# Optimization experiments

Hardware: AMD Instinct MI355X
Metric: run time of the kernel (lower is better)

## Reference

```python
import jax, jax.numpy as jnp
import numpy as np

H = 16  # num_heads
D = 64  # head_dim (latent_dim // num_heads)


def setup_inputs() -> dict:
    key = jax.random.key(0)
    ks = jax.random.split(key, 14)
    B, L, S = 2, 1024, 4096
    input_dim, latent_dim, latent_rank = 2048, 1024, 128
    sc = 0.02
    return {
        "latent": jax.random.normal(ks[0], (B, L, latent_dim), jnp.float32),
        "x": jax.random.normal(ks[1], (B, S, input_dim), jnp.float32),
        "Wq": jax.random.normal(ks[2], (latent_dim, latent_dim), jnp.float32) * sc,
        "bq": jnp.zeros((latent_dim,), jnp.float32),
        "Wc": jax.random.normal(ks[3], (input_dim, latent_rank), jnp.float32) * sc,
        "bc": jnp.zeros((latent_rank,), jnp.float32),
        "Wk": jax.random.normal(ks[4], (latent_rank, latent_dim), jnp.float32) * sc,
        "bk": jnp.zeros((latent_dim,), jnp.float32),
        "Wv": jax.random.normal(ks[5], (latent_rank, latent_dim), jnp.float32) * sc,
        "bv": jnp.zeros((latent_dim,), jnp.float32),
        "Wo": jax.random.normal(ks[6], (latent_dim, latent_dim), jnp.float32) * sc,
        "bo": jnp.zeros((latent_dim,), jnp.float32),
    }


def reference(latent, x, Wq, bq, Wc, bc, Wk, bk, Wv, bv, Wo, bo):
    B, L, latent_dim = latent.shape
    S = x.shape[1]
    # projections
    Q = latent @ Wq + bq                      # [B, L, latent_dim]
    compressed = x @ Wc + bc                  # [B, S, latent_rank] low-rank latent
    K_full = compressed @ Wk + bk             # [B, S, latent_dim]
    V_full = compressed @ Wv + bv             # [B, S, latent_dim]
    # split heads -> [B, H, len, D]
    Qh = Q.reshape(B, L, H, D).transpose(0, 2, 1, 3)
    Kh = K_full.reshape(B, S, H, D).transpose(0, 2, 1, 3)
    Vh = V_full.reshape(B, S, H, D).transpose(0, 2, 1, 3)
    scale = 1.0 / jnp.sqrt(jnp.float32(D))
    scores = jnp.einsum("bhld,bhsd->bhls", Qh, Kh) * scale  # [B,H,L,S]
    attn = jax.nn.softmax(scores, axis=-1)
    ctx = jnp.einsum("bhls,bhsd->bhld", attn, Vh)            # [B,H,L,D]
    ctx = ctx.transpose(0, 2, 1, 3).reshape(B, L, latent_dim)
    return ctx @ Wo + bo
```

## Files before the change

kernel.cpp:

```cpp
#include <hip/hip_runtime.h>
#include <hip/hip_bf16.h>

using bf16x8  = __attribute__((ext_vector_type(8))) short;
using ushort8 = __attribute__((ext_vector_type(8))) unsigned short;
using f32x4   = __attribute__((ext_vector_type(4))) float;

#define DEVINL __device__ __forceinline__

DEVINL unsigned short f2bf(float f) {
    unsigned u = __builtin_bit_cast(unsigned, f);
    u += 0x7FFFu + ((u >> 16) & 1u);
    return (unsigned short)(u >> 16);
}

DEVINL void gload_lds16(const void* g, void* l) {
    __builtin_amdgcn_global_load_lds(
        (const __attribute__((address_space(1))) void*)g,
        (__attribute__((address_space(3))) void*)l, 16, 0, 0);
}

__global__ __launch_bounds__(256) void k_conv(const float* __restrict__ in,
                                              unsigned short* __restrict__ out,
                                              int n8) {
    int i = blockIdx.x * 256 + threadIdx.x;
    if (i >= n8) return;
    const float4* p = (const float4*)in + (size_t)i * 2;
    float4 a = p[0], b = p[1];
    ushort8 r;
    r[0] = f2bf(a.x); r[1] = f2bf(a.y); r[2] = f2bf(a.z); r[3] = f2bf(a.w);
    r[4] = f2bf(b.x); r[5] = f2bf(b.y); r[6] = f2bf(b.z); r[7] = f2bf(b.w);
    *((ushort8*)out + i) = r;
}

__global__ __launch_bounds__(256) void k_convT(const float* __restrict__ in,
                                               unsigned short* __restrict__ out,
                                               int R, int C) {
    __shared__ float t[32][33];
    int c0 = blockIdx.x * 32, r0 = blockIdx.y * 32;
    int tx = threadIdx.x, ty = threadIdx.y;
#pragma unroll
    for (int i = 0; i < 4; i++)
        t[ty + i * 8][tx] = in[(size_t)(r0 + ty + i * 8) * C + c0 + tx];
    __syncthreads();
#pragma unroll
    for (int i = 0; i < 4; i++)
        out[(size_t)(c0 + ty + i * 8) * R + r0 + tx] = f2bf(t[tx][ty + i * 8]);
}

template <int BM, int BN, int OUTBF, int BIASROW>
__global__ __launch_bounds__(256) void k_gemm(const unsigned short* __restrict__ A,
                                              const unsigned short* __restrict__ BT,
                                              const float* __restrict__ bias,
                                              void* __restrict__ Cout,
                                              int M, int N, int K, float scale) {
    constexpr int WM = BM / 2, WN = BN / 2, MI = WM / 16, NI = WN / 16;
    constexpr int CA = BM * 8 / 256, CB = BN * 8 / 256;
    __shared__ unsigned short ls[(BM + BN) * 64];
    unsigned short* lsA = ls;
    unsigned short* lsB = ls + BM * 64;
    const int tid = threadIdx.x, lane = tid & 63, w = tid >> 6;
    const int m0 = blockIdx.y * BM, n0 = blockIdx.x * BN;
    const int mw = (w >> 1) * WM, nw = (w & 1) * WN;
    const int r16 = lane & 15, g4 = lane >> 4;

    f32x4 acc[MI][NI];
#pragma unroll
    for (int a = 0; a < MI; a++)
#pragma unroll
        for (int b = 0; b < NI; b++) acc[a][b] = (f32x4){0.f, 0.f, 0.f, 0.f};

    for (int k0 = 0; k0 < K; k0 += 64) {
#pragma unroll
        for (int i = 0; i < CA; i++) {
            int ch = i * 256 + w * 64 + lane;
            int row = ch >> 3, c = ch & 7;
            gload_lds16(A + (size_t)(m0 + row) * K + k0 + c * 8,
                        lsA + (size_t)(i * 256 + w * 64) * 8);
        }
#pragma unroll
        for (int i = 0; i < CB; i++) {
            int ch = i * 256 + w * 64 + lane;
            int row = ch >> 3, c = ch & 7;
            gload_lds16(BT + (size_t)(n0 + row) * K + k0 + c * 8,
                        lsB + (size_t)(i * 256 + w * 64) * 8);
        }
        __syncthreads();
#pragma unroll
        for (int kk = 0; kk < 2; kk++) {
            bf16x8 af[MI], bfr[NI];
#pragma unroll
            for (int a = 0; a < MI; a++)
                af[a] = *(const bf16x8*)&lsA[(mw + a * 16 + r16) * 64 + kk * 32 + g4 * 8];
#pragma unroll
            for (int b = 0; b < NI; b++)
                bfr[b] = *(const bf16x8*)&lsB[(nw + b * 16 + r16) * 64 + kk * 32 + g4 * 8];
#pragma unroll
            for (int a = 0; a < MI; a++)
#pragma unroll
                for (int b = 0; b < NI; b++)
                    acc[a][b] = __builtin_amdgcn_mfma_f32_16x16x32_bf16(af[a], bfr[b], acc[a][b], 0, 0, 0);
        }
        __syncthreads();
    }
#pragma unroll
    for (int b = 0; b < NI; b++) {
        int col = n0 + nw + b * 16 + r16;
        float bvc = BIASROW ? 0.f : bias[col];
#pragma unroll
        for (int a = 0; a < MI; a++) {
#pragma unroll
            for (int r = 0; r < 4; r++) {
                int row = m0 + mw + a * 16 + g4 * 4 + r;
                float bv = BIASROW ? bias[row] : bvc;
                float v = (acc[a][b][r] + bv) * scale;
                if (OUTBF)
                    ((unsigned short*)Cout)[(size_t)row * N + col] = f2bf(v);
                else
                    ((float*)Cout)[(size_t)row * N + col] = v;
            }
        }
    }
}

__global__ __launch_bounds__(256) void k_attn(const unsigned short* __restrict__ Qb,
                                              const unsigned short* __restrict__ Kb,
                                              const unsigned short* __restrict__ VTb,
                                              float* __restrict__ ctxp,
                                              float2* __restrict__ ML) {
    constexpr int LD = 1024;
    __shared__ unsigned short lsK[2][64 * 64];
    __shared__ unsigned short lsVT[2][64 * 64];
    __shared__ unsigned short lsP[4][16 * 64];
    const int tid = threadIdx.x, lane = tid & 63, w = tid >> 6;
    const int r16 = lane & 15, g4 = lane >> 4;
    const int bh = blockIdx.y, b = bh >> 4, h = bh & 15, z = blockIdx.z;
    const int q0 = blockIdx.x * 64 + w * 16;

    const size_t qbase = ((size_t)b * 1024 + q0 + r16) * LD + h * 64;
    bf16x8 qa0 = *(const bf16x8*)&Qb[qbase + g4 * 8];
    bf16x8 qa1 = *(const bf16x8*)&Qb[qbase + 32 + g4 * 8];

    f32x4 ctxa[4];
#pragma unroll
    for (int d = 0; d < 4; d++) ctxa[d] = (f32x4){0.f, 0.f, 0.f, 0.f};
    float m_run = -1e30f, l_run = 0.f;

    const size_t kbase = (size_t)b * 4096 * LD + h * 64;
    const size_t vtbase = (size_t)bh * 64 * 4096;
    const int lrow = lane >> 3;
    const int lcol = lane & 7;

    auto STAGE = [&](int bufi, int s0) {
#pragma unroll
        for (int i = 0; i < 2; i++) {
            int row = i * 32 + w * 8 + lrow;
            int csrc = lcol ^ (row & 7);
            gload_lds16(Kb + kbase + (size_t)(s0 + row) * LD + csrc * 8,
                        &lsK[bufi][(i * 32 + w * 8) * 64]);
            gload_lds16(VTb + vtbase + (size_t)row * 4096 + s0 + csrc * 8,
                        &lsVT[bufi][(i * 32 + w * 8) * 64]);
        }
    };

    auto COMPUTE = [&](int bufi) {
        f32x4 sc[4];
#pragma unroll
        for (int ni = 0; ni < 4; ni++) sc[ni] = (f32x4){0.f, 0.f, 0.f, 0.f};
        __builtin_amdgcn_s_setprio(1);
#pragma unroll
        for (int kk = 0; kk < 2; kk++) {
            bf16x8 qa = kk ? qa1 : qa0;
#pragma unroll
            for (int ni = 0; ni < 4; ni++) {
                int row = ni * 16 + r16;
                bf16x8 kf = *(const bf16x8*)&lsK[bufi][row * 64 + (((kk * 4 + g4) ^ (row & 7)) * 8)];
                sc[ni] = __builtin_amdgcn_mfma_f32_16x16x32_bf16(kf, qa, sc[ni], 0, 0, 0);
            }
        }
        __builtin_amdgcn_s_setprio(0);

        float pmax = sc[0][0];
#pragma unroll
        for (int ni = 0; ni < 4; ni++)
#pragma unroll
            for (int r = 0; r < 4; r++)
                if (ni || r) pmax = fmaxf(pmax, sc[ni][r]);
        pmax = fmaxf(pmax, __shfl_xor(pmax, 16));
        pmax = fmaxf(pmax, __shfl_xor(pmax, 32));
        float mn = fmaxf(m_run, pmax);
        float corr = exp2f(m_run - mn);
        m_run = mn;
        float p[4][4];
        float rs = 0.f;
#pragma unroll
        for (int ni = 0; ni < 4; ni++)
#pragma unroll
            for (int r = 0; r < 4; r++) {
                p[ni][r] = exp2f(sc[ni][r] - mn);
                rs += p[ni][r];
            }
        rs += __shfl_xor(rs, 16);
        rs += __shfl_xor(rs, 32);
        l_run = l_run * corr + rs;

        float corr4[4];
#pragma unroll
        for (int r = 0; r < 4; r++) corr4[r] = __shfl(corr, g4 * 4 + r);
#pragma unroll
        for (int di = 0; di < 4; di++)
#pragma unroll
            for (int r = 0; r < 4; r++) ctxa[di][r] *= corr4[r];

#pragma unroll
        for (int ni = 0; ni < 4; ni++) {
            int sw = (ni * 2 + (g4 >> 1)) ^ (r16 & 7);
            int base = r16 * 64 + sw * 8 + (g4 & 1) * 4;
#pragma unroll
            for (int pr = 0; pr < 2; pr++) {
                unsigned u;
                asm("v_cvt_pk_bf16_f32 %0, %1, %2"
                    : "=v"(u) : "v"(p[ni][2 * pr]), "v"(p[ni][2 * pr + 1]));
                *(unsigned*)&lsP[w][base + pr * 2] = u;
            }
        }

        __builtin_amdgcn_s_setprio(1);
#pragma unroll
        for (int kk = 0; kk < 2; kk++) {
            bf16x8 pa = *(const bf16x8*)&lsP[w][r16 * 64 + (((kk * 4 + g4) ^ (r16 & 7)) * 8)];
#pragma unroll
            for (int di = 0; di < 4; di++) {
                int row = di * 16 + r16;
                bf16x8 vf = *(const bf16x8*)&lsVT[bufi][row * 64 + (((kk * 4 + g4) ^ (row & 7)) * 8)];
                ctxa[di] = __builtin_amdgcn_mfma_f32_16x16x32_bf16(pa, vf, ctxa[di], 0, 0, 0);
            }
        }
        __builtin_amdgcn_s_setprio(0);
    };

    const int s_base = z * 1024;
    STAGE(0, s_base);
    __syncthreads();
#pragma unroll 1
    for (int tt = 0; tt < 8; tt++) {
        int t0 = tt * 2;
        STAGE(1, s_base + (t0 + 1) * 64);
        COMPUTE(0);
        __syncthreads();
        if (t0 + 2 < 16) STAGE(0, s_base + (t0 + 2) * 64);
        COMPUTE(1);
        __syncthreads();
    }

    float* cp = ctxp + ((size_t)z * 2 + b) * 1024 * 1024;
#pragma unroll
    for (int r = 0; r < 4; r++) {
        int q = q0 + g4 * 4 + r;
#pragma unroll
        for (int di = 0; di < 4; di++)
            cp[(size_t)q * 1024 + h * 64 + di * 16 + r16] = ctxa[di][r];
    }
    if (g4 == 0)
        ML[(((size_t)z * 2 + b) * 16 + h) * 1024 + q0 + r16] = make_float2(m_run, l_run);
}

__global__ __launch_bounds__(256) void k_merge(const float* __restrict__ ctxp,
                                               const float2* __restrict__ ML,
                                               unsigned short* __restrict__ ctx) {
    int gid = blockIdx.x * 256 + threadIdx.x;
    int d8 = gid & 7, h = (gid >> 3) & 15, q = (gid >> 7) & 1023, b = gid >> 17;
    float m[4], l[4];
#pragma unroll
    for (int z = 0; z < 4; z++) {
        float2 e = ML[(((size_t)z * 2 + b) * 16 + h) * 1024 + q];
        m[z] = e.x; l[z] = e.y;
    }
    float M = fmaxf(fmaxf(m[0], m[1]), fmaxf(m[2], m[3]));
    float wz[4], L = 0.f;
#pragma unroll
    for (int z = 0; z < 4; z++) { wz[z] = exp2f(m[z] - M); L += wz[z] * l[z]; }
    float inv = 1.0f / L;
    float o[8];
#pragma unroll
    for (int j = 0; j < 8; j++) o[j] = 0.f;
#pragma unroll
    for (int z = 0; z < 4; z++) {
        const float4* p = (const float4*)(ctxp + ((size_t)z * 2 + b) * 1048576 +
                                          (size_t)q * 1024 + h * 64 + d8 * 8);
        float4 a = p[0], c = p[1];
        o[0] += wz[z] * a.x; o[1] += wz[z] * a.y; o[2] += wz[z] * a.z; o[3] += wz[z] * a.w;
        o[4] += wz[z] * c.x; o[5] += wz[z] * c.y; o[6] += wz[z] * c.z; o[7] += wz[z] * c.w;
    }
    ushort8 r;
#pragma unroll
    for (int j = 0; j < 8; j++) r[j] = f2bf(o[j] * inv);
    *(ushort8*)&ctx[((size_t)b * 1024 + q) * 1024 + h * 64 + d8 * 8] = r;
}

extern "C" void kernel_launch(void* const* d_in, const int* in_sizes, int n_in,
                              void* d_out, int out_size, void* d_ws, size_t ws_size,
                              hipStream_t stream) {
    const float* latent = (const float*)d_in[0];
    const float* x      = (const float*)d_in[1];
    const float* Wq     = (const float*)d_in[2];
    const float* bq     = (const float*)d_in[3];
    const float* Wc     = (const float*)d_in[4];
    const float* bc     = (const float*)d_in[5];
    const float* Wk     = (const float*)d_in[6];
    const float* bk     = (const float*)d_in[7];
    const float* Wv     = (const float*)d_in[8];
    const float* bv     = (const float*)d_in[9];
    const float* Wo     = (const float*)d_in[10];
    const float* bo     = (const float*)d_in[11];
    float* out = (float*)d_out;

    char* ws = (char*)d_ws;
    size_t off = 0;
    auto alloc = [&](size_t shorts) {
        void* p = ws + off;
        off += (shorts * 2 + 255) & ~(size_t)255;
        return (unsigned short*)p;
    };
    unsigned short* lat_bf = alloc(2097152);
    unsigned short* x_bf   = alloc(16777216);
    unsigned short* WqT    = alloc(1048576);
    unsigned short* WcT    = alloc(262144);
    unsigned short* WkT    = alloc(131072);
    unsigned short* WvT    = alloc(131072);
    unsigned short* WoT    = alloc(1048576);
    unsigned short* comp   = alloc(1048576);
    unsigned short* Qb     = alloc(2097152);
    unsigned short* Kb     = alloc(8388608);
    unsigned short* VTb    = alloc(8388608);
    unsigned short* ctxb   = alloc(2097152);
    float*          ctxp   = (float*)alloc(16777216);
    float2*         MLp    = (float2*)alloc(524288);

    dim3 tb(32, 8);
    k_conv<<<2097152 / 2048, 256, 0, stream>>>(latent, lat_bf, 2097152 / 8);
    k_conv<<<16777216 / 2048, 256, 0, stream>>>(x, x_bf, 16777216 / 8);
    k_convT<<<dim3(1024 / 32, 1024 / 32), tb, 0, stream>>>(Wq, WqT, 1024, 1024);
    k_convT<<<dim3(128 / 32, 2048 / 32), tb, 0, stream>>>(Wc, WcT, 2048, 128);
    k_convT<<<dim3(1024 / 32, 128 / 32), tb, 0, stream>>>(Wk, WkT, 128, 1024);
    k_convT<<<dim3(1024 / 32, 128 / 32), tb, 0, stream>>>(Wv, WvT, 128, 1024);
    k_convT<<<dim3(1024 / 32, 1024 / 32), tb, 0, stream>>>(Wo, WoT, 1024, 1024);

    k_gemm<64, 64, 1, 0><<<dim3(2, 128), 256, 0, stream>>>(x_bf, WcT, bc, comp, 8192, 128, 2048, 1.f);
    k_gemm<64, 64, 1, 0><<<dim3(16, 32), 256, 0, stream>>>(lat_bf, WqT, bq, Qb, 2048, 1024, 1024, 0.18033688f);
    k_gemm<128, 128, 1, 0><<<dim3(8, 64), 256, 0, stream>>>(comp, WkT, bk, Kb, 8192, 1024, 128, 1.f);
    k_gemm<64, 64, 1, 1><<<dim3(64, 16), 256, 0, stream>>>(WvT, comp, bv, VTb, 1024, 4096, 128, 1.f);
    k_gemm<64, 64, 1, 1><<<dim3(64, 16), 256, 0, stream>>>(WvT, comp + 4096 * 128, bv,
                                                           VTb + (size_t)16 * 64 * 4096, 1024, 4096, 128, 1.f);
    k_attn<<<dim3(16, 32, 4), 256, 0, stream>>>(Qb, Kb, VTb, ctxp, MLp);
    k_merge<<<1024, 256, 0, stream>>>(ctxp, MLp, ctxb);
    k_gemm<64, 64, 0, 0><<<dim3(16, 32), 256, 0, stream>>>(ctxb, WoT, bo, out, 2048, 1024, 1024, 1.f);
}
```

Measured before the change: 309.0 us.

## Double-buffer GEMM, rebalance attention split, lazy rescale, merge small launches

The GEMM kernel gains a double-buffered LDS pipeline, so the next K tile's global-to-LDS loads overlap the MFMAs on the current one. Attention now splits the sequence three ways instead of four, giving 1536 workgroups, and uses an XCD-aware block index mapping, launch bounds with occupancy 4, and precomputed swizzle offsets. Softmax skips the running-max rescale when the new max grows by less than a threshold, which saves exp and shuffle work but lets exp values grow up to 2^8. Conversion, transpose and V-projection launches are batched into fewer grids to reduce launch overhead, and the compression GEMM uses a 32x128 tile.

```diff
diff --git a/kernel.cpp b/kernel.cpp
--- a/kernel.cpp
+++ b/kernel.cpp
@@ -19,23 +19,34 @@
         (__attribute__((address_space(3))) void*)l, 16, 0, 0);
 }
 
-__global__ __launch_bounds__(256) void k_conv(const float* __restrict__ in,
-                                              unsigned short* __restrict__ out,
-                                              int n8) {
+__global__ __launch_bounds__(256) void k_conv(const float* __restrict__ a,
+                                              unsigned short* __restrict__ oa, int n8a,
+                                              const float* __restrict__ bsrc,
+                                              unsigned short* __restrict__ ob, int n8b) {
     int i = blockIdx.x * 256 + threadIdx.x;
-    if (i >= n8) return;
-    const float4* p = (const float4*)in + (size_t)i * 2;
-    float4 a = p[0], b = p[1];
+    const float* src;
+    unsigned short* dst;
+    if (i < n8a) { src = a + (size_t)i * 8; dst = oa + (size_t)i * 8; }
+    else {
+        int j = i - n8a;
+        if (j >= n8b) return;
+        src = bsrc + (size_t)j * 8; dst = ob + (size_t)j * 8;
+    }
+    float4 A = *(const float4*)src, B = *(const float4*)(src + 4);
     ushort8 r;
-    r[0] = f2bf(a.x); r[1] = f2bf(a.y); r[2] = f2bf(a.z); r[3] = f2bf(a.w);
-    r[4] = f2bf(b.x); r[5] = f2bf(b.y); r[6] = f2bf(b.z); r[7] = f2bf(b.w);
-    *((ushort8*)out + i) = r;
-}
-
-__global__ __launch_bounds__(256) void k_convT(const float* __restrict__ in,
-                                               unsigned short* __restrict__ out,
+    r[0] = f2bf(A.x); r[1] = f2bf(A.y); r[2] = f2bf(A.z); r[3] = f2bf(A.w);
+    r[4] = f2bf(B.x); r[5] = f2bf(B.y); r[6] = f2bf(B.z); r[7] = f2bf(B.w);
+    *(ushort8*)dst = r;
+}
+
+__global__ __launch_bounds__(256) void k_convT(const float* __restrict__ i0,
+                                               unsigned short* __restrict__ o0,
+                                               const float* __restrict__ i1,
+                                               unsigned short* __restrict__ o1,
                                                int R, int C) {
     __shared__ float t[32][33];
+    const float* in = blockIdx.z ? i1 : i0;
+    unsigned short* out = blockIdx.z ? o1 : o0;
     int c0 = blockIdx.x * 32, r0 = blockIdx.y * 32;
     int tx = threadIdx.x, ty = threadIdx.y;
 #pragma unroll
@@ -52,16 +63,16 @@
                                               const unsigned short* __restrict__ BT,
                                               const float* __restrict__ bias,
                                               void* __restrict__ Cout,
-                                              int M, int N, int K, float scale) {
+                                              int M, int N, int K, float scale,
+                                              size_t zA, size_t zB, size_t zC) {
     constexpr int WM = BM / 2, WN = BN / 2, MI = WM / 16, NI = WN / 16;
     constexpr int CA = BM * 8 / 256, CB = BN * 8 / 256;
-    __shared__ unsigned short ls[(BM + BN) * 64];
-    unsigned short* lsA = ls;
-    unsigned short* lsB = ls + BM * 64;
+    __shared__ unsigned short ls[2][(BM + BN) * 64];
     const int tid = threadIdx.x, lane = tid & 63, w = tid >> 6;
-    const int m0 = blockIdx.y * BM, n0 = blockIdx.x * BN;
+    const int m0 = blockIdx.y * BM, n0 = blockIdx.x * BN, zz = blockIdx.z;
     const int mw = (w >> 1) * WM, nw = (w & 1) * WN;
     const int r16 = lane & 15, g4 = lane >> 4;
+    A += zA * zz; BT += zB * zz;
 
     f32x4 acc[MI][NI];
 #pragma unroll
@@ -69,7 +80,9 @@
 #pragma unroll
         for (int b = 0; b < NI; b++) acc[a][b] = (f32x4){0.f, 0.f, 0.f, 0.f};
 
-    for (int k0 = 0; k0 < K; k0 += 64) {
+    auto STAGE = [&](int bufi, int k0) {
+        unsigned short* lsA = ls[bufi];
+        unsigned short* lsB = ls[bufi] + BM * 64;
 #pragma unroll
         for (int i = 0; i < CA; i++) {
             int ch = i * 256 + w * 64 + lane;
@@ -84,7 +97,10 @@
             gload_lds16(BT + (size_t)(n0 + row) * K + k0 + c * 8,
                         lsB + (size_t)(i * 256 + w * 64) * 8);
         }
-        __syncthreads();
+    };
+    auto COMPUTE = [&](int bufi) {
+        const unsigned short* lsA = ls[bufi];
+        const unsigned short* lsB = ls[bufi] + BM * 64;
 #pragma unroll
         for (int kk = 0; kk < 2; kk++) {
             bf16x8 af[MI], bfr[NI];
@@ -100,8 +116,17 @@
                 for (int b = 0; b < NI; b++)
                     acc[a][b] = __builtin_amdgcn_mfma_f32_16x16x32_bf16(af[a], bfr[b], acc[a][b], 0, 0, 0);
         }
+    };
+
+    const int nk = K >> 6;
+    STAGE(0, 0);
+    __syncthreads();
+    for (int t = 0; t < nk; ++t) {
+        if (t + 1 < nk) STAGE((t + 1) & 1, (t + 1) << 6);
+        COMPUTE(t & 1);
         __syncthreads();
     }
+
 #pragma unroll
     for (int b = 0; b < NI; b++) {
         int col = n0 + nw + b * 16 + r16;
@@ -114,27 +139,31 @@
                 float bv = BIASROW ? bias[row] : bvc;
                 float v = (acc[a][b][r] + bv) * scale;
                 if (OUTBF)
-                    ((unsigned short*)Cout)[(size_t)row * N + col] = f2bf(v);
+                    ((unsigned short*)Cout)[zC * zz + (size_t)row * N + col] = f2bf(v);
                 else
-                    ((float*)Cout)[(size_t)row * N + col] = v;
+                    ((float*)Cout)[zC * zz + (size_t)row * N + col] = v;
             }
         }
     }
 }
 
-__global__ __launch_bounds__(256) void k_attn(const unsigned short* __restrict__ Qb,
-                                              const unsigned short* __restrict__ Kb,
-                                              const unsigned short* __restrict__ VTb,
-                                              float* __restrict__ ctxp,
-                                              float2* __restrict__ ML) {
+__global__ __launch_bounds__(256, 4) void k_attn(const unsigned short* __restrict__ Qb,
+                                                 const unsigned short* __restrict__ Kb,
+                                                 const unsigned short* __restrict__ VTb,
+                                                 float* __restrict__ ctxp,
+                                                 float2* __restrict__ ML) {
     constexpr int LD = 1024;
     __shared__ unsigned short lsK[2][64 * 64];
     __shared__ unsigned short lsVT[2][64 * 64];
     __shared__ unsigned short lsP[4][16 * 64];
     const int tid = threadIdx.x, lane = tid & 63, w = tid >> 6;
     const int r16 = lane & 15, g4 = lane >> 4;
-    const int bh = blockIdx.y, b = bh >> 4, h = bh & 15, z = blockIdx.z;
-    const int q0 = blockIdx.x * 64 + w * 16;
+    const int wg = blockIdx.x;
+    const int xcd = wg & 7, t_ = wg >> 3, qi = t_ & 15, gg = t_ >> 4;
+    const int g = gg * 8 + xcd;
+    const int bh = g & 31, z = g >> 5;
+    const int b = bh >> 4, h = bh & 15;
+    const int q0 = qi * 64 + w * 16;
 
     const size_t qbase = ((size_t)b * 1024 + q0 + r16) * LD + h * 64;
     bf16x8 qa0 = *(const bf16x8*)&Qb[qbase + g4 * 8];
@@ -145,21 +174,26 @@
     for (int d = 0; d < 4; d++) ctxa[d] = (f32x4){0.f, 0.f, 0.f, 0.f};
     float m_run = -1e30f, l_run = 0.f;
 
-    const size_t kbase = (size_t)b * 4096 * LD + h * 64;
-    const size_t vtbase = (size_t)bh * 64 * 4096;
-    const int lrow = lane >> 3;
-    const int lcol = lane & 7;
+    const int s7 = r16 & 7;
+    const int offk0 = r16 * 64 + ((g4 ^ s7) << 3);
+    const int offk1 = r16 * 64 + (((g4 + 4) ^ s7) << 3);
+    const int pwb = r16 * 64 + (g4 & 1) * 4;
+    const int c2 = g4 >> 1;
+    const int swn0 = ((0 + c2) ^ s7) << 3, swn1 = ((2 + c2) ^ s7) << 3;
+    const int swn2 = ((4 + c2) ^ s7) << 3, swn3 = ((6 + c2) ^ s7) << 3;
+
+    const int lrow = lane >> 3, lcol = lane & 7;
+    const int csrc = lcol ^ lrow;
+    const unsigned short* gK = Kb + (size_t)b * 4096 * LD + h * 64 +
+                               (size_t)(w * 8 + lrow) * LD + csrc * 8;
+    const unsigned short* gV = VTb + (size_t)bh * 64 * 4096 +
+                               (size_t)(w * 8 + lrow) * 4096 + csrc * 8;
 
     auto STAGE = [&](int bufi, int s0) {
-#pragma unroll
-        for (int i = 0; i < 2; i++) {
-            int row = i * 32 + w * 8 + lrow;
-            int csrc = lcol ^ (row & 7);
-            gload_lds16(Kb + kbase + (size_t)(s0 + row) * LD + csrc * 8,
-                        &lsK[bufi][(i * 32 + w * 8) * 64]);
-            gload_lds16(VTb + vtbase + (size_t)row * 4096 + s0 + csrc * 8,
-                        &lsVT[bufi][(i * 32 + w * 8) * 64]);
-        }
+        gload_lds16(gK + (size_t)s0 * LD, &lsK[bufi][(w * 8) * 64]);
+        gload_lds16(gK + (size_t)(s0 + 32) * LD, &lsK[bufi][(32 + w * 8) * 64]);
+        gload_lds16(gV + s0, &lsVT[bufi][(w * 8) * 64]);
+        gload_lds16(gV + s0 + 32 * 4096, &lsVT[bufi][(32 + w * 8) * 64]);
     };
 
     auto COMPUTE = [&](int bufi) {
@@ -170,10 +204,10 @@
 #pragma unroll
         for (int kk = 0; kk < 2; kk++) {
             bf16x8 qa = kk ? qa1 : qa0;
+            int ofk = kk ? offk1 : offk0;
 #pragma unroll
             for (int ni = 0; ni < 4; ni++) {
-                int row = ni * 16 + r16;
-                bf16x8 kf = *(const bf16x8*)&lsK[bufi][row * 64 + (((kk * 4 + g4) ^ (row & 7)) * 8)];
+                bf16x8 kf = *(const bf16x8*)&lsK[bufi][ni * 1024 + ofk];
                 sc[ni] = __builtin_amdgcn_mfma_f32_16x16x32_bf16(kf, qa, sc[ni], 0, 0, 0);
             }
         }
@@ -187,68 +221,65 @@
                 if (ni || r) pmax = fmaxf(pmax, sc[ni][r]);
         pmax = fmaxf(pmax, __shfl_xor(pmax, 16));
         pmax = fmaxf(pmax, __shfl_xor(pmax, 32));
-        float mn = fmaxf(m_run, pmax);
-        float corr = exp2f(m_run - mn);
-        m_run = mn;
+
+        if (!__all(pmax <= m_run + 8.f)) {
+            float mn = fmaxf(m_run, pmax);
+            float corr = exp2f(m_run - mn);
+            m_run = mn;
+            l_run *= corr;
+            float c4[4];
+#pragma unroll
+            for (int r = 0; r < 4; r++) c4[r] = __shfl(corr, g4 * 4 + r);
+#pragma unroll
+            for (int di = 0; di < 4; di++)
+#pragma unroll
+                for (int r = 0; r < 4; r++) ctxa[di][r] *= c4[r];
+        }
+
         float p[4][4];
         float rs = 0.f;
 #pragma unroll
         for (int ni = 0; ni < 4; ni++)
 #pragma unroll
             for (int r = 0; r < 4; r++) {
-                p[ni][r] = exp2f(sc[ni][r] - mn);
+                p[ni][r] = exp2f(sc[ni][r] - m_run);
                 rs += p[ni][r];
             }
         rs += __shfl_xor(rs, 16);
         rs += __shfl_xor(rs, 32);
-        l_run = l_run * corr + rs;
-
-        float corr4[4];
-#pragma unroll
-        for (int r = 0; r < 4; r++) corr4[r] = __shfl(corr, g4 * 4 + r);
-#pragma unroll
-        for (int di = 0; di < 4; di++)
-#pragma unroll
-            for (int r = 0; r < 4; r++) ctxa[di][r] *= corr4[r];
+        l_run += rs;
 
 #pragma unroll
         for (int ni = 0; ni < 4; ni++) {
-            int sw = (ni * 2 + (g4 >> 1)) ^ (r16 & 7);
-            int base = r16 * 64 + sw * 8 + (g4 & 1) * 4;
-#pragma unroll
-            for (int pr = 0; pr < 2; pr++) {
-                unsigned u;
-                asm("v_cvt_pk_bf16_f32 %0, %1, %2"
-                    : "=v"(u) : "v"(p[ni][2 * pr]), "v"(p[ni][2 * pr + 1]));
-                *(unsigned*)&lsP[w][base + pr * 2] = u;
-            }
+            int sw = ni == 0 ? swn0 : ni == 1 ? swn1 : ni == 2 ? swn2 : swn3;
+            unsigned u0, u1;
+            asm("v_cvt_pk_bf16_f32 %0, %1, %2" : "=v"(u0) : "v"(p[ni][0]), "v"(p[ni][1]));
+            asm("v_cvt_pk_bf16_f32 %0, %1, %2" : "=v"(u1) : "v"(p[ni][2]), "v"(p[ni][3]));
+            *(uint2*)&lsP[w][pwb + sw] = make_uint2(u0, u1);
         }
 
         __builtin_amdgcn_s_setprio(1);
 #pragma unroll
         for (int kk = 0; kk < 2; kk++) {
-            bf16x8 pa = *(const bf16x8*)&lsP[w][r16 * 64 + (((kk * 4 + g4) ^ (r16 & 7)) * 8)];
+            int ofk = kk ? offk1 : offk0;
+            bf16x8 pa = *(const bf16x8*)&lsP[w][ofk];
 #pragma unroll
             for (int di = 0; di < 4; di++) {
-                int row = di * 16 + r16;
-                bf16x8 vf = *(const bf16x8*)&lsVT[bufi][row * 64 + (((kk * 4 + g4) ^ (row & 7)) * 8)];
+                bf16x8 vf = *(const bf16x8*)&lsVT[bufi][di * 1024 + ofk];
                 ctxa[di] = __builtin_amdgcn_mfma_f32_16x16x32_bf16(pa, vf, ctxa[di], 0, 0, 0);
             }
         }
         __builtin_amdgcn_s_setprio(0);
     };
 
-    const int s_base = z * 1024;
-    STAGE(0, s_base);
+    const int t0 = (z * 64) / 3, t1 = ((z + 1) * 64) / 3;
+    STAGE(0, t0 * 64);
     __syncthreads();
 #pragma unroll 1
-    for (int tt = 0; tt < 8; tt++) {
-        int t0 = tt * 2;
-        STAGE(1, s_base + (t0 + 1) * 64);
-        COMPUTE(0);
-        __syncthreads();
-        if (t0 + 2 < 16) STAGE(0, s_base + (t0 + 2) * 64);
-        COMPUTE(1);
+    for (int t = t0; t < t1; ++t) {
+        int pb = (t - t0) & 1;
+        if (t + 1 < t1) STAGE(pb ^ 1, (t + 1) * 64);
+        COMPUTE(pb);
         __syncthreads();
     }
 
@@ -269,22 +300,22 @@
                                                unsigned short* __restrict__ ctx) {
     int gid = blockIdx.x * 256 + threadIdx.x;
     int d8 = gid & 7, h = (gid >> 3) & 15, q = (gid >> 7) & 1023, b = gid >> 17;
-    float m[4], l[4];
-#pragma unroll
-    for (int z = 0; z < 4; z++) {
+    float m[3], l[3];
+#pragma unroll
+    for (int z = 0; z < 3; z++) {
         float2 e = ML[(((size_t)z * 2 + b) * 16 + h) * 1024 + q];
         m[z] = e.x; l[z] = e.y;
     }
-    float M = fmaxf(fmaxf(m[0], m[1]), fmaxf(m[2], m[3]));
-    float wz[4], L = 0.f;
-#pragma unroll
-    for (int z = 0; z < 4; z++) { wz[z] = exp2f(m[z] - M); L += wz[z] * l[z]; }
+    float M = fmaxf(fmaxf(m[0], m[1]), m[2]);
+    float wz[3], L = 0.f;
+#pragma unroll
+    for (int z = 0; z < 3; z++) { wz[z] = exp2f(m[z] - M); L += wz[z] * l[z]; }
     float inv = 1.0f / L;
     float o[8];
 #pragma unroll
     for (int j = 0; j < 8; j++) o[j] = 0.f;
 #pragma unroll
-    for (int z = 0; z < 4; z++) {
+    for (int z = 0; z < 3; z++) {
         const float4* p = (const float4*)(ctxp + ((size_t)z * 2 + b) * 1048576 +
                                           (size_t)q * 1024 + h * 64 + d8 * 8);
         float4 a = p[0], c = p[1];
@@ -333,25 +364,26 @@
     unsigned short* Kb     = alloc(8388608);
     unsigned short* VTb    = alloc(8388608);
     unsigned short* ctxb   = alloc(2097152);
-    float*          ctxp   = (float*)alloc(16777216);
-    float2*         MLp    = (float2*)alloc(524288);
+    float*          ctxp   = (float*)alloc(12582912);
+    float2*         MLp    = (float2*)alloc(393216);
 
     dim3 tb(32, 8);
-    k_conv<<<2097152 / 2048, 256, 0, stream>>>(latent, lat_bf, 2097152 / 8);
-    k_conv<<<16777216 / 2048, 256, 0, stream>>>(x, x_bf, 16777216 / 8);
-    k_convT<<<dim3(1024 / 32, 1024 / 32), tb, 0, stream>>>(Wq, WqT, 1024, 1024);
-    k_convT<<<dim3(128 / 32, 2048 / 32), tb, 0, stream>>>(Wc, WcT, 2048, 128);
-    k_convT<<<dim3(1024 / 32, 128 / 32), tb, 0, stream>>>(Wk, WkT, 128, 1024);
-    k_convT<<<dim3(1024 / 32, 128 / 32), tb, 0, stream>>>(Wv, WvT, 128, 1024);
-    k_convT<<<dim3(1024 / 32, 1024 / 32), tb, 0, stream>>>(Wo, WoT, 1024, 1024);
-
-    k_gemm<64, 64, 1, 0><<<dim3(2, 128), 256, 0, stream>>>(x_bf, WcT, bc, comp, 8192, 128, 2048, 1.f);
-    k_gemm<64, 64, 1, 0><<<dim3(16, 32), 256, 0, stream>>>(lat_bf, WqT, bq, Qb, 2048, 1024, 1024, 0.18033688f);
-    k_gemm<128, 128, 1, 0><<<dim3(8, 64), 256, 0, stream>>>(comp, WkT, bk, Kb, 8192, 1024, 128, 1.f);
-    k_gemm<64, 64, 1, 1><<<dim3(64, 16), 256, 0, stream>>>(WvT, comp, bv, VTb, 1024, 4096, 128, 1.f);
-    k_gemm<64, 64, 1, 1><<<dim3(64, 16), 256, 0, stream>>>(WvT, comp + 4096 * 128, bv,
-                                                           VTb + (size_t)16 * 64 * 4096, 1024, 4096, 128, 1.f);
-    k_attn<<<dim3(16, 32, 4), 256, 0, stream>>>(Qb, Kb, VTb, ctxp, MLp);
+    k_conv<<<9216, 256, 0, stream>>>(latent, lat_bf, 262144, x, x_bf, 2097152);
+    k_convT<<<dim3(32, 32, 2), tb, 0, stream>>>(Wq, WqT, Wo, WoT, 1024, 1024);
+    k_convT<<<dim3(32, 4, 2), tb, 0, stream>>>(Wk, WkT, Wv, WvT, 128, 1024);
+    k_convT<<<dim3(4, 64, 1), tb, 0, stream>>>(Wc, WcT, Wc, WcT, 2048, 128);
+
+    k_gemm<32, 128, 1, 0><<<dim3(1, 256, 1), 256, 0, stream>>>(
+        x_bf, WcT, bc, comp, 8192, 128, 2048, 1.f, 0, 0, 0);
+    k_gemm<64, 64, 1, 0><<<dim3(16, 32, 1), 256, 0, stream>>>(
+        lat_bf, WqT, bq, Qb, 2048, 1024, 1024, 0.18033688f, 0, 0, 0);
+    k_gemm<128, 128, 1, 0><<<dim3(8, 64, 1), 256, 0, stream>>>(
+        comp, WkT, bk, Kb, 8192, 1024, 128, 1.f, 0, 0, 0);
+    k_gemm<64, 64, 1, 1><<<dim3(64, 16, 2), 256, 0, stream>>>(
+        WvT, comp, bv, VTb, 1024, 4096, 128, 1.f,
+        0, (size_t)4096 * 128, (size_t)16 * 64 * 4096);
+    k_attn<<<1536, 256, 0, stream>>>(Qb, Kb, VTb, ctxp, MLp);
     k_merge<<<1024, 256, 0, stream>>>(ctxp, MLp, ctxb);
-    k_gemm<64, 64, 0, 0><<<dim3(16, 32), 256, 0, stream>>>(ctxb, WoT, bo, out, 2048, 1024, 1024, 1.f);
-}
+    k_gemm<64, 64, 0, 0><<<dim3(16, 32, 1), 256, 0, stream>>>(
+        ctxb, WoT, bo, out, 2048, 1024, 1024, 1.f, 0, 0, 0);
+}
```

Measured after the change: 284.1 us. 8.0% less time.
